# Optimization experiments

Measured on AMD Instinct MI355X. Metric: run time of the kernel, lower is better.

The kernel has to match this reference:

```python
import jax, jax.numpy as jnp
import numpy as np

N_ITEMS = 512
TABLE_SAMPLES = 2048
FULL_SIZE = 32768
PADDED_SIZE = 65536
BATCH = 8
N_EVENTS = 64


def setup_inputs() -> dict:
    key = jax.random.key(0)
    k1, k2, k3 = jax.random.split(key, 3)
    selections = jax.random.normal(k1, (BATCH, N_EVENTS, N_ITEMS), dtype=jnp.float32)
    # Envelopes init: uniform(-1,1) * linspace(1,0)**uniform(50,100) per item
    base = jax.random.uniform(k2, (N_ITEMS, TABLE_SAMPLES), minval=-1.0, maxval=1.0)
    exps = jax.random.uniform(jax.random.fold_in(k2, 1), (N_ITEMS, 1), minval=50.0, maxval=100.0)
    ramp = jnp.linspace(1.0, 0.0, TABLE_SAMPLES)[None, :]
    items = (base * ramp ** exps).astype(jnp.float32)
    # postprocess multiplies by uniform(-0.02, 0.02) noise of the interpolated shape
    noise = jax.random.uniform(k3, (BATCH, N_EVENTS, FULL_SIZE), minval=-0.02, maxval=0.02, dtype=jnp.float32)
    return {"selections": selections, "items": items, "noise": noise}


def reference(selections, items, noise):
    # preprocess_items: shift/scale into [0, ~1]
    items = items - items.min()
    items = items / (items.max() + 0.001)

    # select_items(..., type='sparse_softmax'): softmax over items, keep only
    # the max entry (scaled one-hot), then weighted combine against the table.
    sm = jax.nn.softmax(selections, axis=-1)                      # [b, e, n]
    w = jnp.max(sm, axis=-1, keepdims=True)                       # [b, e, 1]
    hard = jax.nn.one_hot(jnp.argmax(sm, axis=-1), sm.shape[-1], dtype=sm.dtype)
    sel = hard * w                                                # sparse one-hot weights
    selected = jnp.einsum('ben,nt->bet', sel, items)              # [b, e, T]

    # interpolate_last_axis: linear interpolation (half-pixel centers) to FULL_SIZE
    in_size = selected.shape[-1]
    pos = (jnp.arange(FULL_SIZE, dtype=jnp.float32) + 0.5) * (in_size / FULL_SIZE) - 0.5
    pos = jnp.clip(pos, 0.0, in_size - 1)
    lo = jnp.floor(pos).astype(jnp.int32)
    hi = jnp.minimum(lo + 1, in_size - 1)
    frac = (pos - lo).astype(selected.dtype)
    amp = selected[..., lo] * (1.0 - frac) + selected[..., hi] * frac  # [b, e, FULL]

    # multiply by noise, pad to PADDED_SIZE
    amp = amp * noise
    pad = jnp.zeros(amp.shape[:-1] + (PADDED_SIZE - FULL_SIZE,), dtype=amp.dtype)
    return jnp.concatenate([amp, pad], axis=-1)                   # [b, e, PADDED]
```

## Files before the change

kernel.cpp:

```cpp
#include <hip/hip_runtime.h>
#include <math.h>

constexpr int N_ITEMS = 512;
constexpr int TS      = 2048;
constexpr int FULL    = 32768;
constexpr int PADDED  = 65536;
constexpr int NPAIR   = 512;

using f4 = __attribute__((ext_vector_type(4))) float;

__device__ __forceinline__ unsigned fenc(float f) {
    unsigned u = __float_as_uint(f);
    return (u & 0x80000000u) ? ~u : (u | 0x80000000u);
}
__device__ __forceinline__ float fdec(unsigned e) {
    return __uint_as_float((e & 0x80000000u) ? (e & 0x7FFFFFFFu) : ~e);
}


__global__ void __launch_bounds__(256) k_prep(const f4* __restrict__ items4,
                                              const float* __restrict__ sel,
                                              unsigned* __restrict__ ws_min,
                                              unsigned* __restrict__ ws_max,
                                              int* __restrict__ ws_idx,
                                              float* __restrict__ ws_w,
                                              float* __restrict__ out) {
    __shared__ unsigned smin[4], smax[4];
    int blk = blockIdx.x;
    int tid = threadIdx.x;

    if (blk < 256) {
        unsigned lmin = 0xFFFFFFFFu, lmax = 0u;
        const int NV = (N_ITEMS * TS) / 4;
        for (int i = blk * 256 + tid; i < NV; i += 256 * 256) {
            f4 v = items4[i];
            unsigned e0 = fenc(v.x), e1 = fenc(v.y), e2 = fenc(v.z), e3 = fenc(v.w);
            lmin = min(min(min(lmin, e0), min(e1, e2)), e3);
            lmax = max(max(max(lmax, e0), max(e1, e2)), e3);
        }
        for (int off = 32; off > 0; off >>= 1) {
            lmin = min(lmin, (unsigned)__shfl_xor((int)lmin, off));
            lmax = max(lmax, (unsigned)__shfl_xor((int)lmax, off));
        }
        int wave = tid >> 6;
        if ((tid & 63) == 0) { smin[wave] = lmin; smax[wave] = lmax; }
        __syncthreads();
        if (tid == 0) {
            ws_min[blk] = min(min(smin[0], smin[1]), min(smin[2], smin[3]));
            ws_max[blk] = max(max(smax[0], smax[1]), max(smax[2], smax[3]));
        }
    } else if (blk < 384) {
        int p    = (blk - 256) * 4 + (tid >> 6);
        int lane = tid & 63;
        const float* s = sel + (size_t)p * N_ITEMS;
        float x[8];
        float vmax = -INFINITY;
        int   imax = 0x7FFFFFFF;
        #pragma unroll
        for (int k = 0; k < 8; ++k) {
            int i = lane + k * 64;
            x[k] = s[i];
            if (x[k] > vmax) { vmax = x[k]; imax = i; }
        }
        for (int off = 32; off > 0; off >>= 1) {
            float ov = __shfl_xor(vmax, off);
            int   oi = __shfl_xor(imax, off);
            if (ov > vmax || (ov == vmax && oi < imax)) { vmax = ov; imax = oi; }
        }
        float se = 0.0f;
        #pragma unroll
        for (int k = 0; k < 8; ++k) se += expf(x[k] - vmax);
        for (int off = 32; off > 0; off >>= 1) se += __shfl_xor(se, off);
        if (lane == 0) { ws_idx[p] = imax; ws_w[p] = 1.0f / se; }
    }

    {
        int p = blk >> 1, h = blk & 1;
        f4* pad4 = (f4*)(out + (size_t)p * PADDED + FULL + (size_t)h * (PADDED - FULL) / 2);
        f4 z = {0.f, 0.f, 0.f, 0.f};
        #pragma unroll
        for (int v = 0; v < 16; ++v)
            __builtin_nontemporal_store(z, &pad4[tid + v * 256]);
    }
}

__global__ void __launch_bounds__(256) k_main(const float* __restrict__ items,
                                              const float* __restrict__ noise,
                                              const unsigned* __restrict__ ws_min,
                                              const unsigned* __restrict__ ws_max,
                                              const int* __restrict__ ws_idx,
                                              const float* __restrict__ ws_w,
                                              float* __restrict__ out) {
    __shared__ float row[TS];
    __shared__ unsigned sred[8];
    __shared__ float s_sb[2];

    int blk = blockIdx.x;
    int p   = blk >> 1;
    int q   = blk & 1;
    int tid = threadIdx.x;

    int idx = ws_idx[p];
    const f4* it4 = (const f4*)(items + (size_t)idx * TS);
    f4 r0 = it4[tid];
    f4 r1 = it4[tid + 256];

    unsigned lmin = ws_min[tid], lmax = ws_max[tid];
    for (int off = 32; off > 0; off >>= 1) {
        lmin = min(lmin, (unsigned)__shfl_xor((int)lmin, off));
        lmax = max(lmax, (unsigned)__shfl_xor((int)lmax, off));
    }
    int wave = tid >> 6;
    if ((tid & 63) == 0) { sred[wave] = lmin; sred[4 + wave] = lmax; }
    __syncthreads();
    if (tid == 0) {
        unsigned m0 = min(min(sred[0], sred[1]), min(sred[2], sred[3]));
        unsigned m1 = max(max(sred[4], sred[5]), max(sred[6], sred[7]));
        float minv  = fdec(m0);
        float maxv  = fdec(m1);
        float denom = (maxv - minv) + 0.001f;
        float scale = ws_w[p] / denom;
        s_sb[0] = scale;
        s_sb[1] = -minv * scale;
    }
    __syncthreads();
    float scale = s_sb[0], bias = s_sb[1];

    row[tid * 4 + 0] = fmaf(r0.x, scale, bias);
    row[tid * 4 + 1] = fmaf(r0.y, scale, bias);
    row[tid * 4 + 2] = fmaf(r0.z, scale, bias);
    row[tid * 4 + 3] = fmaf(r0.w, scale, bias);
    row[(tid + 256) * 4 + 0] = fmaf(r1.x, scale, bias);
    row[(tid + 256) * 4 + 1] = fmaf(r1.y, scale, bias);
    row[(tid + 256) * 4 + 2] = fmaf(r1.z, scale, bias);
    row[(tid + 256) * 4 + 3] = fmaf(r1.w, scale, bias);
    __syncthreads();

    constexpr int CHUNK = FULL / 2;
    const f4* nz4 = (const f4*)(noise + (size_t)p * FULL + (size_t)q * CHUNK);
    f4*       o4  = (f4*)(out + (size_t)p * PADDED + (size_t)q * CHUNK);
    int tbase = q * CHUNK;

    for (int v = tid; v < CHUNK / 4; v += 256) {
        f4 nz = __builtin_nontemporal_load(&nz4[v]);
        f4 o;
        int t0 = tbase + v * 4;
        #pragma unroll
        for (int j = 0; j < 4; ++j) {
            float pos = ((float)(t0 + j) + 0.5f) * 0.0625f - 0.5f;
            pos = fminf(fmaxf(pos, 0.0f), (float)(TS - 1));
            int lo = (int)pos;
            int hi = min(lo + 1, TS - 1);
            float fr = pos - (float)lo;
            float amp = row[lo] * (1.0f - fr) + row[hi] * fr;
            o[j] = amp * nz[j];
        }
        __builtin_nontemporal_store(o, &o4[v]);
    }
}

extern "C" void kernel_launch(void* const* d_in, const int* in_sizes, int n_in,
                              void* d_out, int out_size, void* d_ws, size_t ws_size,
                              hipStream_t stream) {
    const float* sel   = (const float*)d_in[0];
    const float* items = (const float*)d_in[1];
    const float* noise = (const float*)d_in[2];
    float* out = (float*)d_out;

    unsigned* ws_min = (unsigned*)d_ws;
    unsigned* ws_max = (unsigned*)((char*)d_ws + 1024);
    int*      ws_idx = (int*)((char*)d_ws + 2048);
    float*    ws_w   = (float*)((char*)d_ws + 4096);

    hipLaunchKernelGGL(k_prep, dim3(NPAIR * 2), dim3(256), 0, stream,
                       (const f4*)items, sel, ws_min, ws_max, ws_idx, ws_w, out);
    hipLaunchKernelGGL(k_main, dim3(NPAIR * 2), dim3(256), 0, stream,
                       items, noise, ws_min, ws_max, ws_idx, ws_w, out);
}
```

Measured before the change: 40.95 us.

## Split interpolation across four blocks per row and batch noise loads

```diff
diff --git a/kernel.cpp b/kernel.cpp
--- a/kernel.cpp
+++ b/kernel.cpp
@@ -6,6 +6,7 @@
 constexpr int FULL    = 32768;
 constexpr int PADDED  = 65536;
 constexpr int NPAIR   = 512;
+constexpr int SPLIT   = 4;
 
 using f4 = __attribute__((ext_vector_type(4))) float;
 
@@ -84,76 +85,75 @@
     }
 }
 
-__global__ void __launch_bounds__(256) k_main(const float* __restrict__ items,
-                                              const float* __restrict__ noise,
-                                              const unsigned* __restrict__ ws_min,
-                                              const unsigned* __restrict__ ws_max,
-                                              const int* __restrict__ ws_idx,
-                                              const float* __restrict__ ws_w,
-                                              float* __restrict__ out) {
+__global__ void __launch_bounds__(256, 8) k_main(const float* __restrict__ items,
+                                                 const float* __restrict__ noise,
+                                                 const unsigned* __restrict__ ws_min,
+                                                 const unsigned* __restrict__ ws_max,
+                                                 const int* __restrict__ ws_idx,
+                                                 const float* __restrict__ ws_w,
+                                                 float* __restrict__ out) {
     __shared__ float row[TS];
-    __shared__ unsigned sred[8];
-    __shared__ float s_sb[2];
 
-    int blk = blockIdx.x;
-    int p   = blk >> 1;
-    int q   = blk & 1;
-    int tid = threadIdx.x;
+    int blk  = blockIdx.x;
+    int p    = blk >> 2;
+    int q    = blk & 3;
+    int tid  = threadIdx.x;
+    int lane = tid & 63;
 
-    int idx = ws_idx[p];
-    const f4* it4 = (const f4*)(items + (size_t)idx * TS);
-    f4 r0 = it4[tid];
-    f4 r1 = it4[tid + 256];
+    uint4 a = ((const uint4*)ws_min)[lane];
+    uint4 c = ((const uint4*)ws_max)[lane];
+    unsigned gmin = min(min(a.x, a.y), min(a.z, a.w));
+    unsigned gmax = max(max(c.x, c.y), max(c.z, c.w));
+    for (int off = 32; off > 0; off >>= 1) {
+        gmin = min(gmin, (unsigned)__shfl_xor((int)gmin, off));
+        gmax = max(gmax, (unsigned)__shfl_xor((int)gmax, off));
+    }
+    float minv  = fdec(gmin);
+    float maxv  = fdec(gmax);
+    float denom = (maxv - minv) + 0.001f;
+    int   idx   = ws_idx[p];
+    float scale = ws_w[p] / denom;
+    float bias  = -minv * scale;
 
-    unsigned lmin = ws_min[tid], lmax = ws_max[tid];
-    for (int off = 32; off > 0; off >>= 1) {
-        lmin = min(lmin, (unsigned)__shfl_xor((int)lmin, off));
-        lmax = max(lmax, (unsigned)__shfl_xor((int)lmax, off));
-    }
-    int wave = tid >> 6;
-    if ((tid & 63) == 0) { sred[wave] = lmin; sred[4 + wave] = lmax; }
-    __syncthreads();
-    if (tid == 0) {
-        unsigned m0 = min(min(sred[0], sred[1]), min(sred[2], sred[3]));
-        unsigned m1 = max(max(sred[4], sred[5]), max(sred[6], sred[7]));
-        float minv  = fdec(m0);
-        float maxv  = fdec(m1);
-        float denom = (maxv - minv) + 0.001f;
-        float scale = ws_w[p] / denom;
-        s_sb[0] = scale;
-        s_sb[1] = -minv * scale;
+    {
+        const f4* it4 = (const f4*)(items + (size_t)idx * TS);
+        f4 r0 = it4[tid];
+        f4 r1 = it4[tid + 256];
+        row[tid * 4 + 0] = fmaf(r0.x, scale, bias);
+        row[tid * 4 + 1] = fmaf(r0.y, scale, bias);
+        row[tid * 4 + 2] = fmaf(r0.z, scale, bias);
+        row[tid * 4 + 3] = fmaf(r0.w, scale, bias);
+        row[(tid + 256) * 4 + 0] = fmaf(r1.x, scale, bias);
+        row[(tid + 256) * 4 + 1] = fmaf(r1.y, scale, bias);
+        row[(tid + 256) * 4 + 2] = fmaf(r1.z, scale, bias);
+        row[(tid + 256) * 4 + 3] = fmaf(r1.w, scale, bias);
     }
     __syncthreads();
-    float scale = s_sb[0], bias = s_sb[1];
 
-    row[tid * 4 + 0] = fmaf(r0.x, scale, bias);
-    row[tid * 4 + 1] = fmaf(r0.y, scale, bias);
-    row[tid * 4 + 2] = fmaf(r0.z, scale, bias);
-    row[tid * 4 + 3] = fmaf(r0.w, scale, bias);
-    row[(tid + 256) * 4 + 0] = fmaf(r1.x, scale, bias);
-    row[(tid + 256) * 4 + 1] = fmaf(r1.y, scale, bias);
-    row[(tid + 256) * 4 + 2] = fmaf(r1.z, scale, bias);
-    row[(tid + 256) * 4 + 3] = fmaf(r1.w, scale, bias);
-    __syncthreads();
-
-    constexpr int CHUNK = FULL / 2;
+    constexpr int CHUNK = FULL / SPLIT;
     const f4* nz4 = (const f4*)(noise + (size_t)p * FULL + (size_t)q * CHUNK);
     f4*       o4  = (f4*)(out + (size_t)p * PADDED + (size_t)q * CHUNK);
     int tbase = q * CHUNK;
 
-    for (int v = tid; v < CHUNK / 4; v += 256) {
-        f4 nz = __builtin_nontemporal_load(&nz4[v]);
+    f4 nzv[8];
+    #pragma unroll
+    for (int k = 0; k < 8; ++k)
+        nzv[k] = nz4[tid + k * 256];
+
+    #pragma unroll
+    for (int k = 0; k < 8; ++k) {
+        int v  = tid + k * 256;
+        int t0 = tbase + v * 4;
+        float pos0 = ((float)t0 + 0.5f) * 0.0625f - 0.5f;
         f4 o;
-        int t0 = tbase + v * 4;
         #pragma unroll
         for (int j = 0; j < 4; ++j) {
-            float pos = ((float)(t0 + j) + 0.5f) * 0.0625f - 0.5f;
-            pos = fminf(fmaxf(pos, 0.0f), (float)(TS - 1));
-            int lo = (int)pos;
-            int hi = min(lo + 1, TS - 1);
-            float fr = pos - (float)lo;
-            float amp = row[lo] * (1.0f - fr) + row[hi] * fr;
-            o[j] = amp * nz[j];
+            float pj = fminf(fmaxf(pos0 + (float)j * 0.0625f, 0.0f), (float)(TS - 1));
+            int   lj = (int)pj;
+            int   hj = min(lj + 1, TS - 1);
+            float fr = pj - (float)lj;
+            float amp = row[lj] * (1.0f - fr) + row[hj] * fr;
+            o[j] = amp * nzv[k][j];
         }
         __builtin_nontemporal_store(o, &o4[v]);
     }
@@ -174,6 +174,6 @@
 
     hipLaunchKernelGGL(k_prep, dim3(NPAIR * 2), dim3(256), 0, stream,
                        (const f4*)items, sel, ws_min, ws_max, ws_idx, ws_w, out);
-    hipLaunchKernelGGL(k_main, dim3(NPAIR * 2), dim3(256), 0, stream,
+    hipLaunchKernelGGL(k_main, dim3(NPAIR * SPLIT), dim3(256), 0, stream,
                        items, noise, ws_min, ws_max, ws_idx, ws_w, out);
 }
```

Result: faster. 39.17 us (-4.3%).
